# Optimization experiments

Measured on AMD Instinct MI355X. Metric: run time of the kernel, lower is better.

## Reference

```python
import jax, jax.numpy as jnp
import numpy as np

D = 64
NU = 20000
NI = 20000
LU = 50  # user_max_length -> item mailbox length
LI = 50  # item_max_length -> user mailbox length


def setup_inputs() -> dict:
    key = jax.random.key(0)
    ks = jax.random.split(key, 32)
    def p(i, shape):
        return jax.random.normal(ks[i], shape, jnp.float32) * 0.05
    return {
        "user_feat": jax.random.normal(ks[0], (NU, D), jnp.float32),
        "item_feat": jax.random.normal(ks[1], (NI, D), jnp.float32),
        "item_nbr_idx": jax.random.randint(ks[2], (NI, LU), 0, NU, jnp.int32),
        "item_nbr_time": jax.random.randint(ks[3], (NI, LU), 0, 1000000, jnp.int32),
        "user_nbr_idx": jax.random.randint(ks[4], (NU, LI), 0, NI, jnp.int32),
        "user_nbr_time": jax.random.randint(ks[5], (NU, LI), 0, 1000000, jnp.int32),
        "W_user": p(6, (D, D)), "W_item": p(7, (D, D)),
        "u_te": p(8, (LI, D)), "u_te_k": p(9, (LI, D)),
        "i_te": p(10, (LU, D)), "i_te_k": p(11, (LU, D)),
        "gru_u_Wi": p(12, (2, 3 * D, D)), "gru_u_Wh": p(13, (2, 3 * D, D)),
        "gru_u_bi": p(14, (2, 3 * D)), "gru_u_bh": p(15, (2, 3 * D)),
        "gru_i_Wi": p(16, (2, 3 * D, D)), "gru_i_Wh": p(17, (2, 3 * D, D)),
        "gru_i_bi": p(18, (2, 3 * D)), "gru_i_bh": p(19, (2, 3 * D)),
        "gru_lin_u": p(20, (D, 2 * D)), "gru_lin_i": p(21, (D, 2 * D)),
        "agg_u": p(22, (D, 2 * D)), "agg_i": p(23, (D, 2 * D)),
        "upd_u": p(24, (D, 2 * D)), "upd_i": p(25, (D, 2 * D)),
    }


def _gru_dir(x, Wi, Wh, bi, bh):
    # x: [B, L, D] -> outputs [B, L, H]; PyTorch gate order (r, z, n)
    d = Wh.shape[1]
    xw = jnp.einsum('bld,gd->blg', x, Wi) + bi  # [B, L, 3H]
    def step(h, xw_t):
        gh = h @ Wh.T + bh
        r = jax.nn.sigmoid(xw_t[:, :d] + gh[:, :d])
        z = jax.nn.sigmoid(xw_t[:, d:2 * d] + gh[:, d:2 * d])
        n = jnp.tanh(xw_t[:, 2 * d:] + r * gh[:, 2 * d:])
        h = (1.0 - z) * n + z * h
        return h, h
    h0 = jnp.zeros((x.shape[0], d), x.dtype)
    _, hs = jax.lax.scan(step, h0, jnp.swapaxes(xw, 0, 1))
    return jnp.swapaxes(hs, 0, 1)


def _bigru(x, Wi, Wh, bi, bh):
    f = _gru_dir(x, Wi[0], Wh[0], bi[0], bh[0])
    b = _gru_dir(x[:, ::-1], Wi[1], Wh[1], bi[1], bh[1])[:, ::-1]
    return jnp.concatenate([f, b], axis=-1)  # [B, L, 2H]


def _reduce(src_hid, dst_hid, nbr_idx, nbr_time, te, te_k, gWi, gWh, gbi, gbh, glin, agg):
    # Mailbox reduce: gather, time-sort, biGRU, time-embedding attention, last-msg gate.
    mail = src_hid[nbr_idx]                                    # [N, L, D] gather
    L = nbr_time.shape[1]
    order = jnp.argsort(jnp.argsort(nbr_time, axis=1), axis=1)  # rank of each msg
    att_re = L - order - 1                                      # reversed rank
    rnn_order = jnp.argsort(nbr_time, axis=1)
    gru_in = jnp.take_along_axis(mail, rnn_order[..., None], axis=1)
    g = _bigru(gru_in, gWi, gWh, gbi, gbh) @ glin.T             # [N, L, D]
    d = dst_hid.shape[-1]
    e = jnp.sum((te[att_re] + g) * dst_hid[:, None, :], axis=-1) / jnp.sqrt(jnp.float32(d))
    alpha = jax.nn.softmax(e, axis=1)                           # [N, L]
    hid = jnp.sum(alpha[..., None] * (g + te_k[att_re]), axis=1)
    last = jnp.argmax(nbr_time, axis=1)                         # most-recent msg
    last_em = jnp.take_along_axis(mail, last[:, None, None], axis=1)[:, 0]
    return jnp.concatenate([hid, last_em], axis=-1) @ agg.T


def reference(user_feat, item_feat, item_nbr_idx, item_nbr_time, user_nbr_idx, user_nbr_time,
              W_user, W_item, u_te, u_te_k, i_te, i_te_k,
              gru_u_Wi, gru_u_Wh, gru_u_bi, gru_u_bh,
              gru_i_Wi, gru_i_Wh, gru_i_bi, gru_i_bh,
              gru_lin_u, gru_lin_i, agg_u, agg_i, upd_u, upd_i):
    user_hid = user_feat @ W_user.T  # feat_drop is identity at eval
    item_hid = item_feat @ W_item.T
    # 'by' edges: user -> item, reduced per item node
    item_agg = _reduce(user_hid, item_hid, item_nbr_idx, item_nbr_time,
                       i_te, i_te_k, gru_i_Wi, gru_i_Wh, gru_i_bi, gru_i_bh,
                       gru_lin_i, agg_i)
    # 'pby' edges: item -> user, reduced per user node
    user_agg = _reduce(item_hid, user_hid, user_nbr_idx, user_nbr_time,
                       u_te, u_te_k, gru_u_Wi, gru_u_Wh, gru_u_bi, gru_u_bh,
                       gru_lin_u, agg_u)
    user_new = jnp.tanh(jnp.concatenate([user_agg, user_feat], -1) @ upd_u.T)
    item_new = jnp.tanh(jnp.concatenate([item_agg, item_feat], -1) @ upd_i.T)
    return user_new, item_new
```

## Files before the change

kernel.cpp:

```cpp
#include <hip/hip_runtime.h>
#include <math.h>

#define NU 20000
#define NI 20000
#define L  50
#define NODES 32

typedef __attribute__((ext_vector_type(8))) short bfx8;
typedef __attribute__((ext_vector_type(4))) float f32x4;
typedef unsigned short u16;
typedef unsigned char  u8;
typedef unsigned int   u32;

#define OFF_WI    0
#define OFF_H     49152
#define OFF_RID   58368
#define OFF_EF    61696
#define OFF_EB    68352
#define OFF_ORD   75008
#define OFF_ARE   76672
#define OFF_LASTN 78336
#define SMEM_SZ   78464

__device__ __forceinline__ u16 f2bf(float f) {
    u32 u = __float_as_uint(f);
    u = u + 0x7fffu + ((u >> 16) & 1u);
    return (u16)(u >> 16);
}
__device__ __forceinline__ float bf2f(u16 s) {
    return __uint_as_float(((u32)s) << 16);
}
__device__ __forceinline__ u32 cvtpk(float lo, float hi) {
    u32 d;
    asm("v_cvt_pk_bf16_f32 %0, %1, %2" : "=v"(d) : "v"(lo), "v"(hi));
    return d;
}
__device__ __forceinline__ float fsig(float x) {
    return __builtin_amdgcn_rcpf(1.f + __expf(-x));
}
__device__ __forceinline__ float ftanh(float x) {
    float t = __expf(x + x);
    float u = __builtin_amdgcn_rcpf(t + 1.f);
    return __builtin_fmaf(-2.f, u, 1.f);
}
__device__ __forceinline__ bfx8 pack_bf8(const float* p) {
    float4 a = ((const float4*)p)[0];
    float4 b = ((const float4*)p)[1];
    bfx8 r;
    r[0]=(short)f2bf(a.x); r[1]=(short)f2bf(a.y); r[2]=(short)f2bf(a.z); r[3]=(short)f2bf(a.w);
    r[4]=(short)f2bf(b.x); r[5]=(short)f2bf(b.y); r[6]=(short)f2bf(b.z); r[7]=(short)f2bf(b.w);
    return r;
}

__global__ __launch_bounds__(256) void hid_kernel(const float* __restrict__ X,
                                                  const float* __restrict__ W,
                                                  float* __restrict__ Y,
                                                  u16* __restrict__ Yb, int N)
{
    __shared__ float sW[64][65];
    int tid = threadIdx.x;
    for (int i = tid; i < 64 * 64; i += 256) sW[i >> 6][i & 63] = W[i];
    __syncthreads();
    int r = blockIdx.x * 4 + (tid >> 6);
    int d = tid & 63;
    if (r >= N) return;
    const float* x = X + (size_t)r * 64;
    float acc = 0.f;
    #pragma unroll
    for (int k = 0; k < 64; ++k) acc += x[k] * sW[d][k];
    Y[(size_t)r * 64 + d]  = acc;
    Yb[(size_t)r * 64 + d] = f2bf(acc);
}

__global__ __launch_bounds__(256) void upd_kernel(const float* __restrict__ A,
                                                  const float* __restrict__ F,
                                                  const float* __restrict__ U,
                                                  float* __restrict__ out, int N)
{
    __shared__ float sU[64][130];
    int tid = threadIdx.x;
    for (int i = tid; i < 64 * 128; i += 256) sU[i >> 7][i & 127] = U[i];
    __syncthreads();
    int r = blockIdx.x * 4 + (tid >> 6);
    int d = tid & 63;
    if (r >= N) return;
    const float* a = A + (size_t)r * 64;
    const float* f = F + (size_t)r * 64;
    float acc = 0.f;
    #pragma unroll
    for (int k = 0; k < 64; ++k) acc += a[k] * sU[d][k];
    #pragma unroll
    for (int k = 0; k < 64; ++k) acc += f[k] * sU[d][64 + k];
    out[(size_t)r * 64 + d] = tanhf(acc);
}

__global__ __launch_bounds__(256, 1) void reduce32(
    const u16*   __restrict__ srcB,
    const u16*   __restrict__ dstB,
    const int*   __restrict__ nbr_idx,
    const int*   __restrict__ nbr_time,
    const float* __restrict__ te,
    const float* __restrict__ te_k,
    const float* __restrict__ Wi,
    const float* __restrict__ Wh,
    const float* __restrict__ bi,
    const float* __restrict__ bh,
    const float* __restrict__ glin,
    const float* __restrict__ agg,
    float* __restrict__ out)
{
    extern __shared__ __align__(16) char smem[];
    u16*   sWI    = (u16*)(smem + OFF_WI);
    u16*   sRIDp  = (u16*)(smem + OFF_RID);
    float* sEF    = (float*)(smem + OFF_EF);
    float* sEB    = (float*)(smem + OFF_EB);
    u8*    sORD   = (u8*)(smem + OFF_ORD);
    u8*    sARE   = (u8*)(smem + OFF_ARE);
    int*   sLASTN = (int*)(smem + OFF_LASTN);

    const int tid  = threadIdx.x;
    const int lane = tid & 63;
    const int wv   = tid >> 6;
    const int l15  = lane & 15;
    const int grp  = lane >> 4;
    const int lk8  = grp * 8;
    const int nb   = blockIdx.x * NODES;
    const int dir    = wv >> 1;
    const int base16 = (wv & 1) * 16;

    u16* sHw = (u16*)(smem + OFF_H) + wv * 16 * 72;

    int* sTM  = (int*)(smem + OFF_WI);
    int* sNID = sTM + NODES * L;
    for (int p = tid; p < NODES * L; p += 256) {
        sTM[p]  = nbr_time[(size_t)nb * L + p];
        sNID[p] = nbr_idx[(size_t)nb * L + p];
    }
    __syncthreads();
    for (int p = tid; p < NODES * L; p += 256) {
        int m = p / L, l = p - m * L;
        int tl = sTM[p], rank = 0;
        for (int mm = 0; mm < L; ++mm) {
            int tm = sTM[m * L + mm];
            rank += (tm < tl) || (tm == tl && mm < l);
        }
        sORD[m * 52 + rank] = (u8)l;
        sARE[m * 52 + l]    = (u8)(L - 1 - rank);
    }
    if (tid < NODES) {
        int best = 0, bt = sTM[tid * L];
        for (int mm = 1; mm < L; ++mm) {
            int tm = sTM[tid * L + mm];
            if (tm > bt) { bt = tm; best = mm; }
        }
        sLASTN[tid] = sNID[tid * L + best];
    }
    __syncthreads();
    u16* sDST = (u16*)(smem + OFF_H);
    for (int p = tid; p < NODES * L; p += 256) {
        int m = p / L, t = p - m * L;
        sRIDp[m * 52 + t] = (u16)sNID[m * L + sORD[m * 52 + t]];
    }
    for (int p = tid; p < NODES * 64; p += 256) {
        int m = p >> 6, d = p & 63;
        sDST[m * 72 + d] = dstB[(size_t)(nb + m) * 64 + d];
    }
    __syncthreads();

    u16* sGLT = (u16*)(smem + OFF_WI);
    float* sTED = (float*)(smem + OFF_WI + 18432);
    for (int p = tid; p < 8192; p += 256) {
        int d = p >> 7, j = p & 127;
        sGLT[j * 72 + d] = f2bf(glin[(size_t)d * 128 + j]);
    }
    __syncthreads();

    float SV[4][4];
    {
        const u16* drow = sDST + (base16 + l15) * 72;
        bfx8 a0 = *(const bfx8*)(drow + lk8);
        bfx8 a1 = *(const bfx8*)(drow + 32 + lk8);
        #pragma unroll
        for (int nt = 0; nt < 4; ++nt) {
            const u16* gr = sGLT + (dir * 64 + nt * 16 + l15) * 72;
            bfx8 b0 = *(const bfx8*)(gr + lk8);
            bfx8 b1 = *(const bfx8*)(gr + 32 + lk8);
            f32x4 acc = {0.f, 0.f, 0.f, 0.f};
            acc = __builtin_amdgcn_mfma_f32_16x16x32_bf16(a0, b0, acc, 0, 0, 0);
            acc = __builtin_amdgcn_mfma_f32_16x16x32_bf16(a1, b1, acc, 0, 0, 0);
            #pragma unroll
            for (int r = 0; r < 4; ++r) SV[nt][r] = acc[r];
        }
    }
    #pragma unroll
    for (int e = 0; e < 2; ++e) {
        int it = wv * 2 + e, mt = it >> 2, nt = it & 3;
        const u16* drow = sDST + (mt * 16 + l15) * 72;
        bfx8 a0 = *(const bfx8*)(drow + lk8);
        bfx8 a1 = *(const bfx8*)(drow + 32 + lk8);
        int j = nt * 16 + l15;
        const float* tr = te + (size_t)(j < L ? j : 0) * 64;
        bfx8 b0 = pack_bf8(tr + lk8);
        bfx8 b1 = pack_bf8(tr + 32 + lk8);
        f32x4 acc = {0.f, 0.f, 0.f, 0.f};
        acc = __builtin_amdgcn_mfma_f32_16x16x32_bf16(a0, b0, acc, 0, 0, 0);
        acc = __builtin_amdgcn_mfma_f32_16x16x32_bf16(a1, b1, acc, 0, 0, 0);
        #pragma unroll
        for (int r = 0; r < 4; ++r)
            sTED[(mt * 16 + grp * 4 + r) * 68 + j] = acc[r];
    }
    __syncthreads();

    for (int p = tid; p < NODES * L; p += 256) {
        int m = p / L, l = p - m * L;
        sEF[m * 52 + l] = sTED[m * 68 + sARE[m * 52 + l]];
    }
    __syncthreads();

    for (int p = tid; p < 2 * 192 * 64; p += 256) {
        int kk  = p & 63;
        int row = (p >> 6) % 192;
        int dr  = p / (192 * 64);
        int slot = ((kk & 31) >> 3) ^ ((row >> 1) & 3);
        sWI[(((dr * 2 + (kk >> 5)) * 192 + row) << 5) + slot * 8 + (kk & 7)]
            = f2bf(Wi[(size_t)(dr * 192 + row) * 64 + kk]);
    }
    bfx8 whf[12][2];
    float cb[12];
    float pb[4];
    #pragma unroll
    for (int nt = 0; nt < 12; ++nt) {
        const float* wrow = Wh + (size_t)(dir * 192 + nt * 16 + l15) * 64;
        whf[nt][0] = pack_bf8(wrow + lk8);
        whf[nt][1] = pack_bf8(wrow + 32 + lk8);
        float bhv = bh[dir * 192 + nt * 16 + l15];
        cb[nt] = (nt < 8) ? (bi[dir * 192 + nt * 16 + l15] + bhv) : bhv;
    }
    #pragma unroll
    for (int c = 0; c < 4; ++c)
        pb[c] = bi[dir * 192 + 128 + c * 16 + l15];
    __syncthreads();

    f32x4 xcur[12];
    float hp[4][4];
    const int swoff = (grp ^ ((l15 >> 1) & 3)) * 8;
    const u16* wiA = sWI + (((dir * 2 + 0) * 192 + l15) << 5) + swoff;
    const u16* wiB = sWI + (((dir * 2 + 1) * 192 + l15) << 5) + swoff;

    auto produce = [&](bfx8 a0, bfx8 a1) {
        #pragma unroll
        for (int nt = 0; nt < 12; ++nt) {
            bfx8 b0 = *(const bfx8*)(wiA + nt * 512);
            bfx8 b1 = *(const bfx8*)(wiB + nt * 512);
            f32x4 z;
            if (nt >= 8) { float b = pb[nt - 8]; z = (f32x4){b, b, b, b}; }
            else         { z = (f32x4){0.f, 0.f, 0.f, 0.f}; }
            z = __builtin_amdgcn_mfma_f32_16x16x32_bf16(a0, b0, z, 0, 0, 0);
            z = __builtin_amdgcn_mfma_f32_16x16x32_bf16(a1, b1, z, 0, 0, 0);
            xcur[nt] = z;
        }
    };

    auto run_pass = [&](int pass) {
        #pragma unroll
        for (int c = 0; c < 4; ++c)
            #pragma unroll
            for (int r = 0; r < 4; ++r) {
                hp[c][r] = 0.f;
                if (pass == 1) SV[c][r] = 0.f;
                sHw[(grp * 4 + r) * 72 + c * 16 + l15] = 0;
            }
        {
            int tt = dir ? (L - 1) : 0;
            const u16* mrow = srcB + (size_t)sRIDp[(base16 + l15) * 52 + tt] * 64;
            bfx8 a0 = *(const bfx8*)(mrow + lk8);
            bfx8 a1 = *(const bfx8*)(mrow + 32 + lk8);
            produce(a0, a1);
        }
        for (int s = 0; s < L; ++s) {
            bfx8 nA, nB;
            if (s + 1 < L) {
                int tt = dir ? (L - 2 - s) : (s + 1);
                const u16* mrow = srcB + (size_t)sRIDp[(base16 + l15) * 52 + tt] * 64;
                nA = *(const bfx8*)(mrow + lk8);
                nB = *(const bfx8*)(mrow + 32 + lk8);
            }
            bfx8 a0 = *(const bfx8*)(sHw + l15 * 72 + lk8);
            bfx8 a1 = *(const bfx8*)(sHw + l15 * 72 + 32 + lk8);
            int t = dir ? (L - 1 - s) : s;
            float al[4];
            if (pass == 1) {
                #pragma unroll
                for (int r = 0; r < 4; ++r)
                    al[r] = sEF[(base16 + grp * 4 + r) * 52 + t];
            }
            float pe[4] = {0.f, 0.f, 0.f, 0.f};
            #pragma unroll
            for (int c = 0; c < 4; ++c) {
                f32x4 zr  = {cb[c],     cb[c],     cb[c],     cb[c]};
                f32x4 zz4 = {cb[4 + c], cb[4 + c], cb[4 + c], cb[4 + c]};
                f32x4 zn4 = {cb[8 + c], cb[8 + c], cb[8 + c], cb[8 + c]};
                zr  = __builtin_amdgcn_mfma_f32_16x16x32_bf16(a0, whf[c][0],     zr,  0, 0, 0);
                zr  = __builtin_amdgcn_mfma_f32_16x16x32_bf16(a1, whf[c][1],     zr,  0, 0, 0);
                zz4 = __builtin_amdgcn_mfma_f32_16x16x32_bf16(a0, whf[4 + c][0], zz4, 0, 0, 0);
                zz4 = __builtin_amdgcn_mfma_f32_16x16x32_bf16(a1, whf[4 + c][1], zz4, 0, 0, 0);
                zn4 = __builtin_amdgcn_mfma_f32_16x16x32_bf16(a0, whf[8 + c][0], zn4, 0, 0, 0);
                zn4 = __builtin_amdgcn_mfma_f32_16x16x32_bf16(a1, whf[8 + c][1], zn4, 0, 0, 0);
                #pragma unroll
                for (int r = 0; r < 4; ++r) {
                    float rr = fsig(xcur[c][r] + zr[r]);
                    float zz = fsig(xcur[4 + c][r] + zz4[r]);
                    float nn = ftanh(__builtin_fmaf(rr, zn4[r], xcur[8 + c][r]));
                    float h  = __builtin_fmaf(zz, hp[c][r] - nn, nn);
                    hp[c][r] = h;
                    if (pass == 0) pe[r] += h * SV[c][r];
                    else           SV[c][r] += al[r] * h;
                }
            }
            #pragma unroll
            for (int r = 0; r < 4; ++r) {
                u32 p0 = cvtpk(hp[0][r], hp[1][r]);
                u32 p1 = cvtpk(hp[2][r], hp[3][r]);
                u16* hb = sHw + (grp * 4 + r) * 72 + l15;
                hb[0]  = (u16)p0;  hb[16] = (u16)(p0 >> 16);
                hb[32] = (u16)p1;  hb[48] = (u16)(p1 >> 16);
            }
            if (pass == 0) {
                #pragma unroll
                for (int r = 0; r < 4; ++r) {
                    #pragma unroll
                    for (int msk = 1; msk < 16; msk <<= 1)
                        pe[r] += __shfl_xor(pe[r], msk, 64);
                }
                if (l15 == 0) {
                    #pragma unroll
                    for (int r = 0; r < 4; ++r) {
                        int idx = (base16 + grp * 4 + r) * 52 + t;
                        if (dir == 0) sEF[idx] += pe[r];
                        else          sEB[idx]  = pe[r];
                    }
                }
            }
            if (s + 1 < L) produce(nA, nB);
        }
    };

    run_pass(0);
    __syncthreads();

    if (tid < NODES) {
        int m = tid;
        float mx = -1e30f;
        for (int t = 0; t < L; ++t) {
            float v = (sEF[m * 52 + t] + sEB[m * 52 + t]) * 0.125f;
            sEF[m * 52 + t] = v;
            mx = fmaxf(mx, v);
        }
        float sum = 0.f;
        for (int t = 0; t < L; ++t) {
            float ex = __expf(sEF[m * 52 + t] - mx);
            sEF[m * 52 + t] = ex;
            sum += ex;
        }
        float rs = __builtin_amdgcn_rcpf(sum);
        for (int t = 0; t < L; ++t) sEF[m * 52 + t] *= rs;
    }
    __syncthreads();

    run_pass(1);
    __syncthreads();

    u16* sHS   = (u16*)(smem + OFF_WI);
    u16* sA9   = sHS + 32 * 136;
    u16* sTKT  = sA9 + 32 * 136;
    u16* sBETA = (u16*)(smem + OFF_EB);

    #pragma unroll
    for (int c = 0; c < 4; ++c)
        #pragma unroll
        for (int r = 0; r < 4; ++r)
            sHS[(base16 + grp * 4 + r) * 136 + dir * 64 + c * 16 + l15] = f2bf(SV[c][r]);
    if (tid < NODES) {
        for (int t = 0; t < L; ++t)
            sBETA[tid * 72 + sARE[tid * 52 + t]] = f2bf(sEF[tid * 52 + t]);
        for (int j = L; j < 64; ++j) sBETA[tid * 72 + j] = 0;
    }
    for (int p = tid; p < 4096; p += 256) {
        int j = p >> 6, d = p & 63;
        sTKT[d * 72 + j] = (j < L) ? f2bf(te_k[(size_t)j * 64 + d]) : (u16)0;
    }
    for (int p = tid; p < NODES * 64; p += 256) {
        int m = p >> 6, d = p & 63;
        sA9[m * 136 + 64 + d] = srcB[(size_t)sLASTN[m] * 64 + d];
    }
    __syncthreads();

    #pragma unroll
    for (int e = 0; e < 2; ++e) {
        int it = wv * 2 + e, mt = it >> 2, nt = it & 3;
        bfx8 aH[4], aB[2];
        #pragma unroll
        for (int kt = 0; kt < 4; ++kt)
            aH[kt] = *(const bfx8*)(sHS + (mt * 16 + l15) * 136 + kt * 32 + lk8);
        #pragma unroll
        for (int kt = 0; kt < 2; ++kt)
            aB[kt] = *(const bfx8*)(sBETA + (mt * 16 + l15) * 72 + kt * 32 + lk8);
        f32x4 acc = {0.f, 0.f, 0.f, 0.f};
        #pragma unroll
        for (int kt = 0; kt < 4; ++kt) {
            bfx8 b = pack_bf8(glin + (size_t)(nt * 16 + l15) * 128 + kt * 32 + lk8);
            acc = __builtin_amdgcn_mfma_f32_16x16x32_bf16(aH[kt], b, acc, 0, 0, 0);
        }
        #pragma unroll
        for (int kt = 0; kt < 2; ++kt) {
            bfx8 b = *(const bfx8*)(sTKT + (nt * 16 + l15) * 72 + kt * 32 + lk8);
            acc = __builtin_amdgcn_mfma_f32_16x16x32_bf16(aB[kt], b, acc, 0, 0, 0);
        }
        #pragma unroll
        for (int r = 0; r < 4; ++r)
            sA9[(mt * 16 + grp * 4 + r) * 136 + nt * 16 + l15] = f2bf(acc[r]);
    }
    __syncthreads();

    #pragma unroll
    for (int e = 0; e < 2; ++e) {
        int it = wv * 2 + e, mt = it >> 2, nt = it & 3;
        bfx8 aA[4];
        #pragma unroll
        for (int kt = 0; kt < 4; ++kt)
            aA[kt] = *(const bfx8*)(sA9 + (mt * 16 + l15) * 136 + kt * 32 + lk8);
        f32x4 acc = {0.f, 0.f, 0.f, 0.f};
        #pragma unroll
        for (int kt = 0; kt < 4; ++kt) {
            bfx8 b = pack_bf8(agg + (size_t)(nt * 16 + l15) * 128 + kt * 32 + lk8);
            acc = __builtin_amdgcn_mfma_f32_16x16x32_bf16(aA[kt], b, acc, 0, 0, 0);
        }
        #pragma unroll
        for (int r = 0; r < 4; ++r)
            out[(size_t)(nb + mt * 16 + grp * 4 + r) * 64 + nt * 16 + l15] = acc[r];
    }
}

extern "C" void kernel_launch(void* const* d_in, const int* in_sizes, int n_in,
                              void* d_out, int out_size, void* d_ws, size_t ws_size,
                              hipStream_t stream)
{
    const float* user_feat     = (const float*)d_in[0];
    const float* item_feat     = (const float*)d_in[1];
    const int*   item_nbr_idx  = (const int*)d_in[2];
    const int*   item_nbr_time = (const int*)d_in[3];
    const int*   user_nbr_idx  = (const int*)d_in[4];
    const int*   user_nbr_time = (const int*)d_in[5];
    const float* W_user        = (const float*)d_in[6];
    const float* W_item        = (const float*)d_in[7];
    const float* u_te          = (const float*)d_in[8];
    const float* u_te_k        = (const float*)d_in[9];
    const float* i_te          = (const float*)d_in[10];
    const float* i_te_k        = (const float*)d_in[11];
    const float* gru_u_Wi      = (const float*)d_in[12];
    const float* gru_u_Wh      = (const float*)d_in[13];
    const float* gru_u_bi      = (const float*)d_in[14];
    const float* gru_u_bh      = (const float*)d_in[15];
    const float* gru_i_Wi      = (const float*)d_in[16];
    const float* gru_i_Wh      = (const float*)d_in[17];
    const float* gru_i_bi      = (const float*)d_in[18];
    const float* gru_i_bh      = (const float*)d_in[19];
    const float* gru_lin_u     = (const float*)d_in[20];
    const float* gru_lin_i     = (const float*)d_in[21];
    const float* agg_u         = (const float*)d_in[22];
    const float* agg_i         = (const float*)d_in[23];
    const float* upd_u         = (const float*)d_in[24];
    const float* upd_i         = (const float*)d_in[25];

    float* ws       = (float*)d_ws;
    float* user_hid = ws;
    float* item_hid = user_hid + NU * 64;
    float* item_agg = item_hid + NI * 64;
    float* user_agg = item_agg + NI * 64;
    u16*   userB    = (u16*)(user_agg + NU * 64);
    u16*   itemB    = userB + NU * 64;

    (void)hipFuncSetAttribute((const void*)reduce32,
                              hipFuncAttributeMaxDynamicSharedMemorySize, SMEM_SZ);

    hid_kernel<<<NU / 4, 256, 0, stream>>>(user_feat, W_user, user_hid, userB, NU);
    hid_kernel<<<NI / 4, 256, 0, stream>>>(item_feat, W_item, item_hid, itemB, NI);

    reduce32<<<NI / NODES, 256, SMEM_SZ, stream>>>(userB, itemB,
        item_nbr_idx, item_nbr_time, i_te, i_te_k,
        gru_i_Wi, gru_i_Wh, gru_i_bi, gru_i_bh, gru_lin_i, agg_i, item_agg);

    reduce32<<<NU / NODES, 256, SMEM_SZ, stream>>>(itemB, userB,
        user_nbr_idx, user_nbr_time, u_te, u_te_k,
        gru_u_Wi, gru_u_Wh, gru_u_bi, gru_u_bh, gru_lin_u, agg_u, user_agg);

    float* out = (float*)d_out;
    upd_kernel<<<NU / 4, 256, 0, stream>>>(user_agg, user_feat, upd_u, out, NU);
    upd_kernel<<<NI / 4, 256, 0, stream>>>(item_agg, item_feat, upd_i, out + NU * 64, NI);
}
```

Baseline: 1.411 ms.

## Merge both reduce launches, stream pre-converted bf16 GRU weights from global memory

Adds a small kernel that converts the GRU input and hidden weights to bf16 once, pre-scaled by log2e so the gates can use raw exp2. The two reduce launches become one grid. Shared memory is cut from about 78KB to 46KB by dropping the staged weight, glin, te_k and time-embedding tables. Register-held Wh fragments are replaced by per-step loads from global/L2, and launch bounds allow 3 blocks per CU, trading extra cache traffic inside the recurrence for higher occupancy and fewer launches.

```diff
diff --git a/kernel.cpp b/kernel.cpp
--- a/kernel.cpp
+++ b/kernel.cpp
@@ -12,15 +12,17 @@
 typedef unsigned char  u8;
 typedef unsigned int   u32;
 
-#define OFF_WI    0
-#define OFF_H     49152
-#define OFF_RID   58368
-#define OFF_EF    61696
-#define OFF_EB    68352
-#define OFF_ORD   75008
-#define OFF_ARE   76672
-#define OFF_LASTN 78336
-#define SMEM_SZ   78464
+#define LOG2E 1.4426950408889634f
+
+#define OFF_H     0
+#define OFF_RID   9216
+#define OFF_EF    12544
+#define OFF_EB    19200
+#define OFF_ORD   25856
+#define OFF_ARE   27520
+#define OFF_LASTN 29184
+#define OFF_SCR   29312
+#define SMEM_SZ   46720
 
 __device__ __forceinline__ u16 f2bf(float f) {
     u32 u = __float_as_uint(f);
@@ -35,13 +37,16 @@
     asm("v_cvt_pk_bf16_f32 %0, %1, %2" : "=v"(d) : "v"(lo), "v"(hi));
     return d;
 }
-__device__ __forceinline__ float fsig(float x) {
-    return __builtin_amdgcn_rcpf(1.f + __expf(-x));
-}
-__device__ __forceinline__ float ftanh(float x) {
-    float t = __expf(x + x);
-    float u = __builtin_amdgcn_rcpf(t + 1.f);
-    return __builtin_fmaf(-2.f, u, 1.f);
+__device__ __forceinline__ float exp2x(float x) {
+    float r;
+    asm("v_exp_f32 %0, %1" : "=v"(r) : "v"(x));
+    return r;
+}
+__device__ __forceinline__ float fsig2(float a) {
+    return __builtin_amdgcn_rcpf(1.f + exp2x(-a));
+}
+__device__ __forceinline__ float ftanh2(float a) {
+    return __builtin_fmaf(-2.f, __builtin_amdgcn_rcpf(exp2x(a) + 1.f), 1.f);
 }
 __device__ __forceinline__ bfx8 pack_bf8(const float* p) {
     float4 a = ((const float4*)p)[0];
@@ -50,6 +55,20 @@
     r[0]=(short)f2bf(a.x); r[1]=(short)f2bf(a.y); r[2]=(short)f2bf(a.z); r[3]=(short)f2bf(a.w);
     r[4]=(short)f2bf(b.x); r[5]=(short)f2bf(b.y); r[6]=(short)f2bf(b.z); r[7]=(short)f2bf(b.w);
     return r;
+}
+
+__global__ __launch_bounds__(256) void convw_kernel(
+    const float* __restrict__ Wi_i, const float* __restrict__ Wh_i,
+    const float* __restrict__ Wi_u, const float* __restrict__ Wh_u,
+    u16* __restrict__ o)
+{
+    int idx = blockIdx.x * 256 + threadIdx.x;
+    int m   = idx / 24576, rem = idx - m * 24576;
+    int row = rem >> 6;
+    int gate = (row % 192) >> 6;
+    const float* src = (m == 0) ? Wi_i : (m == 1) ? Wh_i : (m == 2) ? Wi_u : Wh_u;
+    float sc = (gate < 2) ? LOG2E : (2.f * LOG2E);
+    o[idx] = f2bf(src[rem] * sc);
 }
 
 __global__ __launch_bounds__(256) void hid_kernel(const float* __restrict__ X,
@@ -94,23 +113,21 @@
     out[(size_t)r * 64 + d] = tanhf(acc);
 }
 
-__global__ __launch_bounds__(256, 1) void reduce32(
-    const u16*   __restrict__ srcB,
-    const u16*   __restrict__ dstB,
-    const int*   __restrict__ nbr_idx,
-    const int*   __restrict__ nbr_time,
-    const float* __restrict__ te,
-    const float* __restrict__ te_k,
-    const float* __restrict__ Wi,
-    const float* __restrict__ Wh,
-    const float* __restrict__ bi,
-    const float* __restrict__ bh,
-    const float* __restrict__ glin,
-    const float* __restrict__ agg,
-    float* __restrict__ out)
+__global__ __launch_bounds__(256, 3) void reduce_all(
+    const u16*   __restrict__ userB,
+    const u16*   __restrict__ itemB,
+    const int*   __restrict__ i_idx,  const int*   __restrict__ i_time,
+    const int*   __restrict__ u_idx,  const int*   __restrict__ u_time,
+    const float* __restrict__ i_te,   const float* __restrict__ i_tek,
+    const float* __restrict__ u_te,   const float* __restrict__ u_tek,
+    const u16*   __restrict__ WB,
+    const float* __restrict__ i_bi,   const float* __restrict__ i_bh,
+    const float* __restrict__ u_bi,   const float* __restrict__ u_bh,
+    const float* __restrict__ i_glin, const float* __restrict__ u_glin,
+    const float* __restrict__ i_agg,  const float* __restrict__ u_agg,
+    float* __restrict__ item_out, float* __restrict__ user_out, int nbi)
 {
     extern __shared__ __align__(16) char smem[];
-    u16*   sWI    = (u16*)(smem + OFF_WI);
     u16*   sRIDp  = (u16*)(smem + OFF_RID);
     float* sEF    = (float*)(smem + OFF_EF);
     float* sEB    = (float*)(smem + OFF_EB);
@@ -118,19 +135,35 @@
     u8*    sARE   = (u8*)(smem + OFF_ARE);
     int*   sLASTN = (int*)(smem + OFF_LASTN);
 
+    const bool isU = (int)blockIdx.x >= nbi;
+    const int  bid = isU ? ((int)blockIdx.x - nbi) : (int)blockIdx.x;
+    const u16*   srcB     = isU ? itemB  : userB;
+    const u16*   dstB     = isU ? userB  : itemB;
+    const int*   nbr_idx  = isU ? u_idx  : i_idx;
+    const int*   nbr_time = isU ? u_time : i_time;
+    const float* te       = isU ? u_te   : i_te;
+    const float* tek      = isU ? u_tek  : i_tek;
+    const u16*   WiB      = WB + (size_t)(isU ? 2 : 0) * 24576;
+    const u16*   WhB      = WB + (size_t)(isU ? 3 : 1) * 24576;
+    const float* bi       = isU ? u_bi   : i_bi;
+    const float* bh       = isU ? u_bh   : i_bh;
+    const float* glin     = isU ? u_glin : i_glin;
+    const float* agg      = isU ? u_agg  : i_agg;
+    float*       out      = isU ? user_out : item_out;
+
     const int tid  = threadIdx.x;
     const int lane = tid & 63;
     const int wv   = tid >> 6;
     const int l15  = lane & 15;
     const int grp  = lane >> 4;
     const int lk8  = grp * 8;
-    const int nb   = blockIdx.x * NODES;
+    const int nb   = bid * NODES;
     const int dir    = wv >> 1;
     const int base16 = (wv & 1) * 16;
 
     u16* sHw = (u16*)(smem + OFF_H) + wv * 16 * 72;
 
-    int* sTM  = (int*)(smem + OFF_WI);
+    int* sTM  = (int*)(smem + OFF_SCR);
     int* sNID = sTM + NODES * L;
     for (int p = tid; p < NODES * L; p += 256) {
         sTM[p]  = nbr_time[(size_t)nb * L + p];
@@ -156,6 +189,7 @@
         sLASTN[tid] = sNID[tid * L + best];
     }
     __syncthreads();
+
     u16* sDST = (u16*)(smem + OFF_H);
     for (int p = tid; p < NODES * L; p += 256) {
         int m = p / L, t = p - m * L;
@@ -164,14 +198,6 @@
     for (int p = tid; p < NODES * 64; p += 256) {
         int m = p >> 6, d = p & 63;
         sDST[m * 72 + d] = dstB[(size_t)(nb + m) * 64 + d];
-    }
-    __syncthreads();
-
-    u16* sGLT = (u16*)(smem + OFF_WI);
-    float* sTED = (float*)(smem + OFF_WI + 18432);
-    for (int p = tid; p < 8192; p += 256) {
-        int d = p >> 7, j = p & 127;
-        sGLT[j * 72 + d] = f2bf(glin[(size_t)d * 128 + j]);
     }
     __syncthreads();
 
@@ -182,9 +208,13 @@
         bfx8 a1 = *(const bfx8*)(drow + 32 + lk8);
         #pragma unroll
         for (int nt = 0; nt < 4; ++nt) {
-            const u16* gr = sGLT + (dir * 64 + nt * 16 + l15) * 72;
-            bfx8 b0 = *(const bfx8*)(gr + lk8);
-            bfx8 b1 = *(const bfx8*)(gr + 32 + lk8);
+            int j = dir * 64 + nt * 16 + l15;
+            bfx8 b0, b1;
+            #pragma unroll
+            for (int i = 0; i < 8; ++i) {
+                b0[i] = (short)f2bf(glin[(size_t)(lk8 + i) * 128 + j]);
+                b1[i] = (short)f2bf(glin[(size_t)(32 + lk8 + i) * 128 + j]);
+            }
             f32x4 acc = {0.f, 0.f, 0.f, 0.f};
             acc = __builtin_amdgcn_mfma_f32_16x16x32_bf16(a0, b0, acc, 0, 0, 0);
             acc = __builtin_amdgcn_mfma_f32_16x16x32_bf16(a1, b1, acc, 0, 0, 0);
@@ -193,8 +223,8 @@
         }
     }
     #pragma unroll
-    for (int e = 0; e < 2; ++e) {
-        int it = wv * 2 + e, mt = it >> 2, nt = it & 3;
+    for (int e2 = 0; e2 < 2; ++e2) {
+        int it = wv * 2 + e2, mt = it >> 2, nt = it & 3;
         const u16* drow = sDST + (mt * 16 + l15) * 72;
         bfx8 a0 = *(const bfx8*)(drow + lk8);
         bfx8 a1 = *(const bfx8*)(drow + 32 + lk8);
@@ -205,53 +235,37 @@
         f32x4 acc = {0.f, 0.f, 0.f, 0.f};
         acc = __builtin_amdgcn_mfma_f32_16x16x32_bf16(a0, b0, acc, 0, 0, 0);
         acc = __builtin_amdgcn_mfma_f32_16x16x32_bf16(a1, b1, acc, 0, 0, 0);
-        #pragma unroll
-        for (int r = 0; r < 4; ++r)
-            sTED[(mt * 16 + grp * 4 + r) * 68 + j] = acc[r];
-    }
-    __syncthreads();
-
-    for (int p = tid; p < NODES * L; p += 256) {
-        int m = p / L, l = p - m * L;
-        sEF[m * 52 + l] = sTED[m * 68 + sARE[m * 52 + l]];
-    }
-    __syncthreads();
-
-    for (int p = tid; p < 2 * 192 * 64; p += 256) {
-        int kk  = p & 63;
-        int row = (p >> 6) % 192;
-        int dr  = p / (192 * 64);
-        int slot = ((kk & 31) >> 3) ^ ((row >> 1) & 3);
-        sWI[(((dr * 2 + (kk >> 5)) * 192 + row) << 5) + slot * 8 + (kk & 7)]
-            = f2bf(Wi[(size_t)(dr * 192 + row) * 64 + kk]);
-    }
-    bfx8 whf[12][2];
-    float cb[12];
-    float pb[4];
+        if (j < L) {
+            #pragma unroll
+            for (int r = 0; r < 4; ++r) {
+                int m = mt * 16 + grp * 4 + r;
+                sEF[m * 52 + sORD[m * 52 + (L - 1 - j)]] = acc[r];
+            }
+        }
+    }
+
+    float cb[12], pb[4];
     #pragma unroll
     for (int nt = 0; nt < 12; ++nt) {
-        const float* wrow = Wh + (size_t)(dir * 192 + nt * 16 + l15) * 64;
-        whf[nt][0] = pack_bf8(wrow + lk8);
-        whf[nt][1] = pack_bf8(wrow + 32 + lk8);
         float bhv = bh[dir * 192 + nt * 16 + l15];
-        cb[nt] = (nt < 8) ? (bi[dir * 192 + nt * 16 + l15] + bhv) : bhv;
+        cb[nt] = (nt < 8) ? (bi[dir * 192 + nt * 16 + l15] + bhv) * LOG2E
+                          : bhv * (2.f * LOG2E);
     }
     #pragma unroll
     for (int c = 0; c < 4; ++c)
-        pb[c] = bi[dir * 192 + 128 + c * 16 + l15];
+        pb[c] = bi[dir * 192 + 128 + c * 16 + l15] * (2.f * LOG2E);
     __syncthreads();
 
     f32x4 xcur[12];
     float hp[4][4];
-    const int swoff = (grp ^ ((l15 >> 1) & 3)) * 8;
-    const u16* wiA = sWI + (((dir * 2 + 0) * 192 + l15) << 5) + swoff;
-    const u16* wiB = sWI + (((dir * 2 + 1) * 192 + l15) << 5) + swoff;
+    const u16* wiP = WiB + (((size_t)dir * 192 + l15) << 6) + lk8;
+    const u16* whP = WhB + (((size_t)dir * 192 + l15) << 6) + lk8;
 
     auto produce = [&](bfx8 a0, bfx8 a1) {
         #pragma unroll
         for (int nt = 0; nt < 12; ++nt) {
-            bfx8 b0 = *(const bfx8*)(wiA + nt * 512);
-            bfx8 b1 = *(const bfx8*)(wiB + nt * 512);
+            bfx8 b0 = *(const bfx8*)(wiP + nt * 1024);
+            bfx8 b1 = *(const bfx8*)(wiP + nt * 1024 + 32);
             f32x4 z;
             if (nt >= 8) { float b = pb[nt - 8]; z = (f32x4){b, b, b, b}; }
             else         { z = (f32x4){0.f, 0.f, 0.f, 0.f}; }
@@ -273,11 +287,10 @@
         {
             int tt = dir ? (L - 1) : 0;
             const u16* mrow = srcB + (size_t)sRIDp[(base16 + l15) * 52 + tt] * 64;
-            bfx8 a0 = *(const bfx8*)(mrow + lk8);
-            bfx8 a1 = *(const bfx8*)(mrow + 32 + lk8);
-            produce(a0, a1);
+            produce(*(const bfx8*)(mrow + lk8), *(const bfx8*)(mrow + 32 + lk8));
         }
         for (int s = 0; s < L; ++s) {
+            asm volatile("" : "+v"(wiP), "+v"(whP));
             bfx8 nA, nB;
             if (s + 1 < L) {
                 int tt = dir ? (L - 2 - s) : (s + 1);
@@ -297,20 +310,26 @@
             float pe[4] = {0.f, 0.f, 0.f, 0.f};
             #pragma unroll
             for (int c = 0; c < 4; ++c) {
+                bfx8 br0 = *(const bfx8*)(whP + c * 1024);
+                bfx8 br1 = *(const bfx8*)(whP + c * 1024 + 32);
+                bfx8 bz0 = *(const bfx8*)(whP + (4 + c) * 1024);
+                bfx8 bz1 = *(const bfx8*)(whP + (4 + c) * 1024 + 32);
+                bfx8 bn0 = *(const bfx8*)(whP + (8 + c) * 1024);
+                bfx8 bn1 = *(const bfx8*)(whP + (8 + c) * 1024 + 32);
                 f32x4 zr  = {cb[c],     cb[c],     cb[c],     cb[c]};
                 f32x4 zz4 = {cb[4 + c], cb[4 + c], cb[4 + c], cb[4 + c]};
                 f32x4 zn4 = {cb[8 + c], cb[8 + c], cb[8 + c], cb[8 + c]};
-                zr  = __builtin_amdgcn_mfma_f32_16x16x32_bf16(a0, whf[c][0],     zr,  0, 0, 0);
-                zr  = __builtin_amdgcn_mfma_f32_16x16x32_bf16(a1, whf[c][1],     zr,  0, 0, 0);
-                zz4 = __builtin_amdgcn_mfma_f32_16x16x32_bf16(a0, whf[4 + c][0], zz4, 0, 0, 0);
-                zz4 = __builtin_amdgcn_mfma_f32_16x16x32_bf16(a1, whf[4 + c][1], zz4, 0, 0, 0);
-                zn4 = __builtin_amdgcn_mfma_f32_16x16x32_bf16(a0, whf[8 + c][0], zn4, 0, 0, 0);
-                zn4 = __builtin_amdgcn_mfma_f32_16x16x32_bf16(a1, whf[8 + c][1], zn4, 0, 0, 0);
+                zr  = __builtin_amdgcn_mfma_f32_16x16x32_bf16(a0, br0, zr,  0, 0, 0);
+                zr  = __builtin_amdgcn_mfma_f32_16x16x32_bf16(a1, br1, zr,  0, 0, 0);
+                zz4 = __builtin_amdgcn_mfma_f32_16x16x32_bf16(a0, bz0, zz4, 0, 0, 0);
+                zz4 = __builtin_amdgcn_mfma_f32_16x16x32_bf16(a1, bz1, zz4, 0, 0, 0);
+                zn4 = __builtin_amdgcn_mfma_f32_16x16x32_bf16(a0, bn0, zn4, 0, 0, 0);
+                zn4 = __builtin_amdgcn_mfma_f32_16x16x32_bf16(a1, bn1, zn4, 0, 0, 0);
                 #pragma unroll
                 for (int r = 0; r < 4; ++r) {
-                    float rr = fsig(xcur[c][r] + zr[r]);
-                    float zz = fsig(xcur[4 + c][r] + zz4[r]);
-                    float nn = ftanh(__builtin_fmaf(rr, zn4[r], xcur[8 + c][r]));
+                    float rr = fsig2(xcur[c][r] + zr[r]);
+                    float zz = fsig2(xcur[4 + c][r] + zz4[r]);
+                    float nn = ftanh2(__builtin_fmaf(rr, zn4[r], xcur[8 + c][r]));
                     float h  = __builtin_fmaf(zz, hp[c][r] - nn, nn);
                     hp[c][r] = h;
                     if (pass == 0) pe[r] += h * SV[c][r];
@@ -370,9 +389,8 @@
     run_pass(1);
     __syncthreads();
 
-    u16* sHS   = (u16*)(smem + OFF_WI);
+    u16* sHS   = (u16*)(smem + OFF_SCR);
     u16* sA9   = sHS + 32 * 136;
-    u16* sTKT  = sA9 + 32 * 136;
     u16* sBETA = (u16*)(smem + OFF_EB);
 
     #pragma unroll
@@ -385,10 +403,6 @@
             sBETA[tid * 72 + sARE[tid * 52 + t]] = f2bf(sEF[tid * 52 + t]);
         for (int j = L; j < 64; ++j) sBETA[tid * 72 + j] = 0;
     }
-    for (int p = tid; p < 4096; p += 256) {
-        int j = p >> 6, d = p & 63;
-        sTKT[d * 72 + j] = (j < L) ? f2bf(te_k[(size_t)j * 64 + d]) : (u16)0;
-    }
     for (int p = tid; p < NODES * 64; p += 256) {
         int m = p >> 6, d = p & 63;
         sA9[m * 136 + 64 + d] = srcB[(size_t)sLASTN[m] * 64 + d];
@@ -396,8 +410,8 @@
     __syncthreads();
 
     #pragma unroll
-    for (int e = 0; e < 2; ++e) {
-        int it = wv * 2 + e, mt = it >> 2, nt = it & 3;
+    for (int e2 = 0; e2 < 2; ++e2) {
+        int it = wv * 2 + e2, mt = it >> 2, nt = it & 3;
         bfx8 aH[4], aB[2];
         #pragma unroll
         for (int kt = 0; kt < 4; ++kt)
@@ -413,7 +427,12 @@
         }
         #pragma unroll
         for (int kt = 0; kt < 2; ++kt) {
-            bfx8 b = *(const bfx8*)(sTKT + (nt * 16 + l15) * 72 + kt * 32 + lk8);
+            bfx8 b;
+            #pragma unroll
+            for (int i = 0; i < 8; ++i) {
+                int j = kt * 32 + lk8 + i;
+                b[i] = (short)((j < L) ? f2bf(tek[(size_t)j * 64 + nt * 16 + l15]) : (u16)0);
+            }
             acc = __builtin_amdgcn_mfma_f32_16x16x32_bf16(aB[kt], b, acc, 0, 0, 0);
         }
         #pragma unroll
@@ -423,8 +442,8 @@
     __syncthreads();
 
     #pragma unroll
-    for (int e = 0; e < 2; ++e) {
-        int it = wv * 2 + e, mt = it >> 2, nt = it & 3;
+    for (int e2 = 0; e2 < 2; ++e2) {
+        int it = wv * 2 + e2, mt = it >> 2, nt = it & 3;
         bfx8 aA[4];
         #pragma unroll
         for (int kt = 0; kt < 4; ++kt)
@@ -479,20 +498,24 @@
     float* user_agg = item_agg + NI * 64;
     u16*   userB    = (u16*)(user_agg + NU * 64);
     u16*   itemB    = userB + NU * 64;
-
-    (void)hipFuncSetAttribute((const void*)reduce32,
+    u16*   WB       = itemB + NI * 64;
+
+    (void)hipFuncSetAttribute((const void*)reduce_all,
                               hipFuncAttributeMaxDynamicSharedMemorySize, SMEM_SZ);
 
+    convw_kernel<<<384, 256, 0, stream>>>(gru_i_Wi, gru_i_Wh, gru_u_Wi, gru_u_Wh, WB);
     hid_kernel<<<NU / 4, 256, 0, stream>>>(user_feat, W_user, user_hid, userB, NU);
     hid_kernel<<<NI / 4, 256, 0, stream>>>(item_feat, W_item, item_hid, itemB, NI);
 
-    reduce32<<<NI / NODES, 256, SMEM_SZ, stream>>>(userB, itemB,
-        item_nbr_idx, item_nbr_time, i_te, i_te_k,
-        gru_i_Wi, gru_i_Wh, gru_i_bi, gru_i_bh, gru_lin_i, agg_i, item_agg);
-
-    reduce32<<<NU / NODES, 256, SMEM_SZ, stream>>>(itemB, userB,
-        user_nbr_idx, user_nbr_time, u_te, u_te_k,
-        gru_u_Wi, gru_u_Wh, gru_u_bi, gru_u_bh, gru_lin_u, agg_u, user_agg);
+    const int NBI = NI / NODES;
+    reduce_all<<<NBI + NU / NODES, 256, SMEM_SZ, stream>>>(
+        userB, itemB,
+        item_nbr_idx, item_nbr_time, user_nbr_idx, user_nbr_time,
+        i_te, i_te_k, u_te, u_te_k,
+        WB,
+        gru_i_bi, gru_i_bh, gru_u_bi, gru_u_bh,
+        gru_lin_i, gru_lin_u, agg_i, agg_u,
+        item_agg, user_agg, NBI);
 
     float* out = (float*)d_out;
     upd_kernel<<<NU / 4, 256, 0, stream>>>(user_agg, user_feat, upd_u, out, NU);
```

After: 3.475 ms. 2.46x slower.
